# Kernel tuning notes

Measured on AMD Instinct MI355X. Metric: run time of the kernel, lower is better.

The kernel has to match this reference:

```python
import jax, jax.numpy as jnp
import numpy as np

# Static config (matches init_kwargs)
B, T, D = 4, 2048, 1024
E = 8            # num_experts
K = 2            # top_k
S = 1            # num_shared_experts
H = 1408         # expert_hidden_dim = round_to(4*1024//(K+S), 64)
N = B * T        # 8192 tokens
CAPACITY = 2560  # ceil(1.25 * K * N / E)
AUX_COEF = 0.01


def setup_inputs() -> dict:
    key = jax.random.key(0)
    ks = jax.random.split(key, 6)
    s = 1024 ** -0.5
    return {
        "x": jax.random.normal(ks[0], (B, T, D), jnp.float32),
        "router_weight": jax.random.normal(ks[1], (E, D), jnp.float32) * 0.02,
        "w_fc": jax.random.normal(ks[2], (E, D, H), jnp.float32) * s,
        "w_proj": jax.random.normal(ks[3], (E, H, D), jnp.float32) * s,
        "ws_fc": jax.random.normal(ks[4], (S, D, H), jnp.float32) * s,
        "ws_proj": jax.random.normal(ks[5], (S, H, D), jnp.float32) * s,
    }


def reference(x, router_weight, w_fc, w_proj, ws_fc, ws_proj):
    x_flat = x.reshape(N, D)

    # Shared experts: relu(x @ ws_fc)^2 @ ws_proj, summed over S experts
    h_s = jnp.square(jax.nn.relu(jnp.einsum("nd,sdh->snh", x_flat, ws_fc)))
    shared_out = jnp.einsum("snh,shd->nd", h_s, ws_proj)

    # Router: softmax in fp32, top-k, renormalize
    router_logits = x_flat @ router_weight.T                 # [N, E]
    routing_probs = jax.nn.softmax(router_logits.astype(jnp.float32), axis=-1)
    topk_probs, topk_idx = jax.lax.top_k(routing_probs, K)   # [N, K]
    topk_probs = topk_probs / (jnp.sum(topk_probs, axis=-1, keepdims=True) + 1e-9)
    topk_probs = topk_probs.astype(x.dtype)

    # Aux load-balancing loss (f uses top-1 assignment, no grad)
    f = jax.lax.stop_gradient(
        jnp.mean(jax.nn.one_hot(topk_idx[:, 0], E, dtype=routing_probs.dtype), axis=0))
    p = jnp.mean(routing_probs, axis=0)
    aux_loss = AUX_COEF * float(E) * jnp.sum(f * p)

    # Capacity-based dispatch: stable sort assignments by expert id
    flat_idx = topk_idx.reshape(-1)                          # [N*K]
    flat_probs = topk_probs.reshape(-1)                      # [N*K]
    flat_tok = jnp.repeat(jnp.arange(N, dtype=jnp.int32), K)  # [N*K]
    order = jnp.argsort(flat_idx, stable=True)
    sorted_idx = flat_idx[order]
    sorted_tok = flat_tok[order]
    sorted_probs = flat_probs[order]

    counts = jnp.zeros((E,), jnp.int32).at[flat_idx].add(1)
    starts = jnp.concatenate([jnp.zeros((1,), jnp.int32), jnp.cumsum(counts[:-1])])
    pos_within = jnp.arange(N * K, dtype=jnp.int32) - starts[sorted_idx]
    keep = (pos_within < CAPACITY).astype(x.dtype)
    pos_clamped = jnp.minimum(pos_within, CAPACITY - 1)
    slot = sorted_idx * CAPACITY + pos_clamped               # [N*K] -> E*CAPACITY buffer

    # Scatter tokens into per-expert capacity buffers (dropped tokens zeroed by keep)
    expert_inputs = jnp.zeros((E * CAPACITY, D), x.dtype).at[slot].add(
        x_flat[sorted_tok] * keep[:, None])
    expert_inputs = expert_inputs.reshape(E, CAPACITY, D)

    # Grouped expert FFN: relu(.)^2 MLP per expert
    hidden = jnp.square(jax.nn.relu(jnp.einsum("ecd,edh->ech", expert_inputs, w_fc)))
    expert_output = jnp.einsum("ech,ehd->ecd", hidden, w_proj).reshape(E * CAPACITY, D)

    # Gather + weighted scatter-combine back to tokens
    gathered = expert_output[slot]                           # [N*K, D]
    weighted = gathered * (sorted_probs * keep)[:, None]
    routed_out = jnp.zeros((N, D), x.dtype).at[sorted_tok].add(weighted)

    y = (routed_out + shared_out).reshape(B, T, D)
    return y, aux_loss
```

## Files before the change

### kernel.cpp

```cpp
#include <hip/hip_runtime.h>


#define NTOK 8192
#define DDIM 1024
#define HDIM 1408
#define CAP  2560
#define NROWS (NTOK + 8*CAP)
#define YN   8388608

typedef __bf16 bf16x8 __attribute__((ext_vector_type(8)));
typedef float  f32x4  __attribute__((ext_vector_type(4)));

typedef __attribute__((address_space(1))) void gvoid_t;
typedef __attribute__((address_space(3))) void svoid_t;

static __device__ __forceinline__ void load_lds16(const void* g, void* l) {
  __builtin_amdgcn_global_load_lds((gvoid_t*)g, (svoid_t*)l, 16, 0, 0);
}

__global__ __launch_bounds__(256) void zero_kernel(float* __restrict__ y,
                                                   float* __restrict__ psum,
                                                   int* __restrict__ fcnt) {
  size_t idx = (size_t)blockIdx.x * 256 + threadIdx.x;
  float4 z = make_float4(0.f, 0.f, 0.f, 0.f);
  float4* p = (float4*)y;
#pragma unroll
  for (int j = 0; j < 4; ++j) p[idx + (size_t)j * 524288] = z;
  if (idx == 0) {
    y[YN] = 0.f;
    for (int e = 0; e < 8; ++e) { psum[e] = 0.f; fcnt[e] = 0; }
  }
}

__global__ __launch_bounds__(256) void convx_kernel(const float* __restrict__ in,
                                                    __bf16* __restrict__ out) {
  size_t i = ((size_t)blockIdx.x * 256 + threadIdx.x) * 8;
  float4 a = *(const float4*)(in + i);
  float4 b = *(const float4*)(in + i + 4);
  bf16x8 o;
  o[0] = (__bf16)a.x; o[1] = (__bf16)a.y; o[2] = (__bf16)a.z; o[3] = (__bf16)a.w;
  o[4] = (__bf16)b.x; o[5] = (__bf16)b.y; o[6] = (__bf16)b.z; o[7] = (__bf16)b.w;
  *(bf16x8*)(out + i) = o;
}

__global__ __launch_bounds__(256) void tconv_kernel(const float* __restrict__ in,
                                                    __bf16* __restrict__ out, int R, int C) {
  __shared__ float t[32][33];
  size_t mo = (size_t)blockIdx.z * R * C;
  const float* ip = in + mo;
  __bf16* op = out + mo;
  int c0 = blockIdx.x * 32, r0 = blockIdx.y * 32;
  int tx = threadIdx.x, ty = threadIdx.y;
#pragma unroll
  for (int k2 = 0; k2 < 4; ++k2)
    t[ty + k2 * 8][tx] = ip[(size_t)(r0 + ty + k2 * 8) * C + c0 + tx];
  __syncthreads();
#pragma unroll
  for (int k2 = 0; k2 < 4; ++k2)
    op[(size_t)(c0 + ty + k2 * 8) * R + r0 + tx] = (__bf16)t[tx][ty + k2 * 8];
}

__global__ __launch_bounds__(256) void router_kernel(
    const float* __restrict__ x, const float* __restrict__ rw,
    int2* __restrict__ e01, float2* __restrict__ p01,
    int* __restrict__ tok_row, float* __restrict__ scale_row,
    float* __restrict__ psum, int* __restrict__ fcnt) {
  __shared__ float rwl[8 * 1024];
  __shared__ float ps[8];
  __shared__ int fc[8];
  int tid = threadIdx.x;
  if (tid < 8) { ps[tid] = 0.f; fc[tid] = 0; }
  float4* rl4 = (float4*)rwl;
  const float4* rg4 = (const float4*)rw;
#pragma unroll
  for (int j = 0; j < 8; ++j) rl4[tid + 256 * j] = rg4[tid + 256 * j];
  __syncthreads();
  int lane = tid & 63, wid = tid >> 6;
  for (int it = 0; it < 8; ++it) {
    int t = blockIdx.x * 32 + wid * 8 + it;
    const float4* xt = (const float4*)(x + (size_t)t * DDIM);
    float a[8];
#pragma unroll
    for (int e = 0; e < 8; ++e) a[e] = 0.f;
#pragma unroll
    for (int jj = 0; jj < 4; ++jj) {
      float4 v = xt[lane * 4 + jj];
#pragma unroll
      for (int e = 0; e < 8; ++e) {
        float4 w = rl4[e * 256 + lane * 4 + jj];
        a[e] += v.x * w.x + v.y * w.y + v.z * w.z + v.w * w.w;
      }
    }
#pragma unroll
    for (int off = 32; off >= 1; off >>= 1)
#pragma unroll
      for (int e = 0; e < 8; ++e) a[e] += __shfl_xor(a[e], off);
    if (lane == 0) {
      int am = 0; float m = a[0];
      for (int e = 1; e < 8; ++e) if (a[e] > m) { m = a[e]; am = e; }
      float s = 0.f, ex[8];
      for (int e = 0; e < 8; ++e) { ex[e] = expf(a[e] - m); s += ex[e]; }
      float inv = 1.f / s;
      int am2 = -1; float m2 = -3.4e38f;
      for (int e = 0; e < 8; ++e) if (e != am && a[e] > m2) { m2 = a[e]; am2 = e; }
      float p0 = ex[am] * inv, p1 = ex[am2] * inv;
      float rn = 1.f / (p0 + p1 + 1e-9f);
      e01[t] = make_int2(am, am2);
      p01[t] = make_float2(p0 * rn, p1 * rn);
      tok_row[t] = t;
      scale_row[t] = 1.f;
      atomicAdd(&fc[am], 1);
      for (int e = 0; e < 8; ++e) atomicAdd(&ps[e], ex[e] * inv);
    }
  }
  __syncthreads();
  if (tid < 8) { atomicAdd(&psum[tid], ps[tid]); atomicAdd(&fcnt[tid], fc[tid]); }
}

__global__ __launch_bounds__(256) void dispatch_kernel(
    const int2* __restrict__ e01, const float2* __restrict__ p01,
    int* __restrict__ tok_row, float* __restrict__ scale_row, int* __restrict__ counts) {
  __shared__ int lcnt[256][8];
  int tid = threadIdx.x;
  int my[8];
#pragma unroll
  for (int e = 0; e < 8; ++e) my[e] = 0;
  int base = tid * 64;
  for (int j = 0; j < 64; ++j) {
    int ent = base + j; int t = ent >> 1;
    int2 ee = e01[t];
    int ex = (ent & 1) ? ee.y : ee.x;
    my[ex]++;
  }
#pragma unroll
  for (int e = 0; e < 8; ++e) lcnt[tid][e] = my[e];
  __syncthreads();
  if (tid < 8) {
    int run = 0;
    for (int i = 0; i < 256; ++i) { int c = lcnt[i][tid]; lcnt[i][tid] = run; run += c; }
    counts[tid] = run < CAP ? run : CAP;
  }
  __syncthreads();
  int offs[8];
#pragma unroll
  for (int e = 0; e < 8; ++e) offs[e] = lcnt[tid][e];
  for (int j = 0; j < 64; ++j) {
    int ent = base + j; int t = ent >> 1; int k = ent & 1;
    int2 ee = e01[t];
    int ex = k ? ee.y : ee.x;
    float pr = k ? p01[t].y : p01[t].x;
    int pos = offs[ex]++;
    if (pos < CAP) {
      int row = NTOK + ex * CAP + pos;
      tok_row[row] = t;
      scale_row[row] = pr;
    }
  }
}

template <int BM, int BN, int KD, int NDT, int WNV, bool GATHER, int EPI>
__global__ __launch_bounds__(512, 2) void gemm_kernel(
    const __bf16* __restrict__ A, const __bf16* __restrict__ B,
    __bf16* __restrict__ Hout, float* __restrict__ Yout,
    const int* __restrict__ counts, const int* __restrict__ tok_row,
    const float* __restrict__ scale_row) {
  constexpr int NCT = NDT / BN;
  constexpr int T = KD / 32;
  constexpr int AI = BM / 16;
  constexpr int BI = BN / 16;
  constexpr int LI = (AI + BI) / 8;
  constexpr int SH = NTOK / BM;
  constexpr int ET = CAP / BM;
  int nwg = gridDim.x;
  int lin = (blockIdx.x & 7) * (nwg >> 3) + (blockIdx.x >> 3);
  int rem = lin % (4 * NCT);
  int rt = (lin / (4 * NCT)) * 4 + (rem & 3);
  int ct = rem >> 2;

  int g, i0, rowbase;
  if (rt < SH) { g = 8; rowbase = 0; i0 = rt * BM; }
  else { int r = rt - SH; g = r / ET; i0 = (r % ET) * BM; rowbase = NTOK + g * CAP; }
  int cnt = (g == 8) ? NTOK : counts[g];
  if (i0 >= cnt) return;

  __shared__ __align__(16) __bf16 As[4][BM * 32];
  __shared__ __align__(16) __bf16 Bs[4][BN * 32];
  __shared__ int   toksL[BM];
  __shared__ float sclL[BM];

  int tid = threadIdx.x, lane = tid & 63, wid = tid >> 6;

  if (tid < BM) {
    int i = i0 + tid; if (i > cnt - 1) i = cnt - 1;
    toksL[tid] = tok_row[rowbase + i];
    if (EPI == 2) sclL[tid] = scale_row[rowbase + i];
  }
  __syncthreads();

  const char* gsrc[LI];
  int ldsoff[LI];
  bool isA[LI];
  const char* Bg = (const char*)B + (size_t)g * NDT * KD * 2;
#pragma unroll
  for (int q = 0; q < LI; ++q) {
    int j = wid * LI + q;
    int rsub = lane >> 2;
    int chunk = lane & 3;
    if (j < AI) {
      int row = j * 16 + rsub;
      size_t arow = GATHER ? (size_t)toksL[row] : (size_t)(rowbase + i0 + row);
      int csw = chunk ^ ((row >> 1) & 3);
      gsrc[q] = (const char*)A + arow * (size_t)(KD * 2) + csw * 16;
      ldsoff[q] = j * 1024;
      isA[q] = true;
    } else {
      int jb = j - AI;
      int row = jb * 16 + rsub;
      int ib = ct * BN + row;
      int csw = chunk ^ ((row >> 1) & 3);
      gsrc[q] = Bg + (size_t)ib * (KD * 2) + csw * 16;
      ldsoff[q] = jb * 1024;
      isA[q] = false;
    }
  }

  f32x4 acc[4][4];
#pragma unroll
  for (int m2 = 0; m2 < 4; ++m2)
#pragma unroll
    for (int n2 = 0; n2 < 4; ++n2) acc[m2][n2] = f32x4{0.f, 0.f, 0.f, 0.f};

  int wr = wid / WNV, wc = wid % WNV;
  int rdA[4], rdB[4];
#pragma unroll
  for (int m2 = 0; m2 < 4; ++m2) {
    int row = wr * 64 + m2 * 16 + (lane & 15);
    int cs = (lane >> 4) ^ ((row >> 1) & 3);
    rdA[m2] = row * 64 + cs * 16;
  }
#pragma unroll
  for (int n2 = 0; n2 < 4; ++n2) {
    int row = wc * 64 + n2 * 16 + (lane & 15);
    int cs = (lane >> 4) ^ ((row >> 1) & 3);
    rdB[n2] = row * 64 + cs * 16;
  }

  auto stage = [&](int buf, int t) {
#pragma unroll
    for (int q = 0; q < LI; ++q) {
      char* l = (char*)(isA[q] ? &As[buf][0] : &Bs[buf][0]) + ldsoff[q];
      load_lds16(gsrc[q] + (size_t)t * 64, l);
    }
  };
  auto compute = [&](int buf) {
    bf16x8 af[4], bfr[4];
#pragma unroll
    for (int m2 = 0; m2 < 4; ++m2)
      af[m2] = *(const bf16x8*)((const char*)&As[buf][0] + rdA[m2]);
#pragma unroll
    for (int n2 = 0; n2 < 4; ++n2)
      bfr[n2] = *(const bf16x8*)((const char*)&Bs[buf][0] + rdB[n2]);
    __builtin_amdgcn_s_setprio(1);
#pragma unroll
    for (int m2 = 0; m2 < 4; ++m2)
#pragma unroll
      for (int n2 = 0; n2 < 4; ++n2)
        acc[m2][n2] = __builtin_amdgcn_mfma_f32_16x16x32_bf16(af[m2], bfr[n2], acc[m2][n2], 0, 0, 0);
    __builtin_amdgcn_s_setprio(0);
  };
  auto syncstep = [&](int n) {
    if (n == 0)      asm volatile("s_waitcnt vmcnt(0)" ::: "memory");
    else if (n == 3) asm volatile("s_waitcnt vmcnt(3)" ::: "memory");
    else             asm volatile("s_waitcnt vmcnt(6)" ::: "memory");
    __builtin_amdgcn_s_barrier();
    __builtin_amdgcn_sched_barrier(0);
  };

  stage(0, 0);
  stage(1, 1);
  stage(2, 2);
  syncstep(6);
#pragma unroll 4
  for (int t = 0; t < T - 3; ++t) {
    stage((t + 3) & 3, t + 3);
    compute(t & 3);
    syncstep(6);
  }
  compute((T - 3) & 3);
  syncstep(3);
  compute((T - 2) & 3);
  syncstep(0);
  compute((T - 1) & 3);

#pragma unroll
  for (int m2 = 0; m2 < 4; ++m2) {
    int rb = wr * 64 + m2 * 16 + ((lane >> 4) << 2);
#pragma unroll
    for (int n2 = 0; n2 < 4; ++n2) {
      int col = ct * BN + wc * 64 + n2 * 16 + (lane & 15);
#pragma unroll
      for (int r = 0; r < 4; ++r) {
        int grow = i0 + rb + r;
        if (grow < cnt) {
          float v = acc[m2][n2][r];
          if constexpr (EPI == 1) {
            v = fmaxf(v, 0.f);
            Hout[(size_t)(rowbase + grow) * NDT + col] = (__bf16)(v * v);
          } else {
            atomicAdd(&Yout[(size_t)toksL[rb + r] * NDT + col], v * sclL[rb + r]);
          }
        }
      }
    }
  }
}

__global__ void aux_kernel(const float* __restrict__ psum, const int* __restrict__ fcnt,
                           float* __restrict__ out) {
  float s = 0.f;
  for (int e = 0; e < 8; ++e) s += ((float)fcnt[e] / 8192.f) * (psum[e] / 8192.f);
  *out = 0.08f * s;
}

extern "C" void kernel_launch(void* const* d_in, const int* in_sizes, int n_in,
                              void* d_out, int out_size, void* d_ws, size_t ws_size,
                              hipStream_t stream) {
  const float* x      = (const float*)d_in[0];
  const float* rw     = (const float*)d_in[1];
  const float* wfc    = (const float*)d_in[2];
  const float* wproj  = (const float*)d_in[3];
  const float* wsfc   = (const float*)d_in[4];
  const float* wsproj = (const float*)d_in[5];
  float* y = (float*)d_out;

  char* ws = (char*)d_ws;
  size_t off = 0;
  auto alloc = [&](size_t bytes) {
    void* p = ws + off;
    off += (bytes + 1023) & ~(size_t)1023;
    return p;
  };
  __bf16* xbf      = (__bf16*)alloc((size_t)NTOK * DDIM * 2);
  __bf16* B1       = (__bf16*)alloc((size_t)9 * HDIM * DDIM * 2);
  __bf16* B2       = (__bf16*)alloc((size_t)9 * DDIM * HDIM * 2);
  __bf16* H        = (__bf16*)alloc((size_t)NROWS * HDIM * 2);
  int*    tok_row  = (int*)alloc((size_t)NROWS * 4);
  float*  scale_row= (float*)alloc((size_t)NROWS * 4);
  int2*   e01      = (int2*)alloc((size_t)NTOK * 8);
  float2* p01      = (float2*)alloc((size_t)NTOK * 8);
  int*    counts   = (int*)alloc(1024);
  float*  psum     = (float*)alloc(1024);
  int*    fcnt     = (int*)alloc(1024);
  (void)ws_size; (void)out_size; (void)in_sizes; (void)n_in;

  zero_kernel<<<2048, 256, 0, stream>>>(y, psum, fcnt);
  convx_kernel<<<4096, 256, 0, stream>>>(x, xbf);
  dim3 tb(32, 8);
  tconv_kernel<<<dim3(44, 32, 8), tb, 0, stream>>>(wfc, B1, 1024, 1408);
  tconv_kernel<<<dim3(44, 32, 1), tb, 0, stream>>>(wsfc, B1 + (size_t)8 * HDIM * DDIM, 1024, 1408);
  tconv_kernel<<<dim3(32, 44, 8), tb, 0, stream>>>(wproj, B2, 1408, 1024);
  tconv_kernel<<<dim3(32, 44, 1), tb, 0, stream>>>(wsproj, B2 + (size_t)8 * DDIM * HDIM, 1408, 1024);
  router_kernel<<<256, 256, 0, stream>>>(x, rw, e01, p01, tok_row, scale_row, psum, fcnt);
  dispatch_kernel<<<1, 256, 0, stream>>>(e01, p01, tok_row, scale_row, counts);
  gemm_kernel<256, 128, 1024, 1408, 2, true, 1><<<1232, 512, 0, stream>>>(
      xbf, B1, H, nullptr, counts, tok_row, scale_row);
  gemm_kernel<128, 256, 1408, 1024, 4, false, 2><<<896, 512, 0, stream>>>(
      H, B2, nullptr, y, counts, tok_row, scale_row);
  aux_kernel<<<1, 1, 0, stream>>>(psum, fcnt, y + YN);
}
```

Measured before the change: 363.4 us.

## Use 256x256 GEMM tiles and pad expert hidden dim to 1536

Both grouped expert GEMMs now use 256x256 block tiles, with each wave computing a 64x128 sub-tile, so there is more data reuse per LDS load and fewer workgroups. The hidden dimension is padded from 1408 to 1536 so it divides evenly by 256. A new kernel zeroes the padded rows of the first weight matrix, and the transpose kernel gains output stride parameters. The padding adds about 9% extra MFMA work. The larger tiles double LDS per block and the accumulator register count, which may lower occupancy. The padded K columns of the second weight matrix are never initialized, so correctness relies on the zeroed hidden columns multiplying that unset memory without producing NaN.

Result: slower. 387.7 us (+6.7%).

```diff
diff --git a/kernel.cpp b/kernel.cpp
--- a/kernel.cpp
+++ b/kernel.cpp
@@ -4,6 +4,7 @@
 #define NTOK 8192
 #define DDIM 1024
 #define HDIM 1408
+#define HP   1536
 #define CAP  2560
 #define NROWS (NTOK + 8*CAP)
 #define YN   8388608
@@ -30,6 +31,14 @@
     y[YN] = 0.f;
     for (int e = 0; e < 8; ++e) { psum[e] = 0.f; fcnt[e] = 0; }
   }
+}
+
+__global__ __launch_bounds__(256) void zpad_kernel(__bf16* __restrict__ B1) {
+  int idx = blockIdx.x * 256 + threadIdx.x;
+  int e = idx >> 14;
+  int w = idx & 16383;
+  size_t off = (size_t)e * HP * 1024 + (size_t)(HDIM + (w >> 7)) * 1024 + (w & 127) * 8;
+  *(float4*)(B1 + off) = make_float4(0.f, 0.f, 0.f, 0.f);
 }
 
 __global__ __launch_bounds__(256) void convx_kernel(const float* __restrict__ in,
@@ -44,11 +53,11 @@
 }
 
 __global__ __launch_bounds__(256) void tconv_kernel(const float* __restrict__ in,
-                                                    __bf16* __restrict__ out, int R, int C) {
+                                                    __bf16* __restrict__ out,
+                                                    int R, int C, int OS, size_t zs) {
   __shared__ float t[32][33];
-  size_t mo = (size_t)blockIdx.z * R * C;
-  const float* ip = in + mo;
-  __bf16* op = out + mo;
+  const float* ip = in + (size_t)blockIdx.z * R * C;
+  __bf16* op = out + (size_t)blockIdx.z * zs;
   int c0 = blockIdx.x * 32, r0 = blockIdx.y * 32;
   int tx = threadIdx.x, ty = threadIdx.y;
 #pragma unroll
@@ -57,7 +66,7 @@
   __syncthreads();
 #pragma unroll
   for (int k2 = 0; k2 < 4; ++k2)
-    op[(size_t)(c0 + ty + k2 * 8) * R + r0 + tx] = (__bf16)t[tx][ty + k2 * 8];
+    op[(size_t)(c0 + ty + k2 * 8) * OS + r0 + tx] = (__bf16)t[tx][ty + k2 * 8];
 }
 
 __global__ __launch_bounds__(256) void router_kernel(
@@ -158,17 +167,17 @@
   }
 }
 
-template <int BM, int BN, int KD, int NDT, int WNV, bool GATHER, int EPI>
+template <int KD, int NDT, bool GATHER, int EPI>
 __global__ __launch_bounds__(512, 2) void gemm_kernel(
     const __bf16* __restrict__ A, const __bf16* __restrict__ B,
     __bf16* __restrict__ Hout, float* __restrict__ Yout,
     const int* __restrict__ counts, const int* __restrict__ tok_row,
     const float* __restrict__ scale_row) {
+  constexpr int BM = 256, BN = 256;
   constexpr int NCT = NDT / BN;
   constexpr int T = KD / 32;
   constexpr int AI = BM / 16;
-  constexpr int BI = BN / 16;
-  constexpr int LI = (AI + BI) / 8;
+  constexpr int LI = 4;
   constexpr int SH = NTOK / BM;
   constexpr int ET = CAP / BM;
   int nwg = gridDim.x;
@@ -224,14 +233,14 @@
     }
   }
 
-  f32x4 acc[4][4];
+  f32x4 acc[4][8];
 #pragma unroll
   for (int m2 = 0; m2 < 4; ++m2)
 #pragma unroll
-    for (int n2 = 0; n2 < 4; ++n2) acc[m2][n2] = f32x4{0.f, 0.f, 0.f, 0.f};
-
-  int wr = wid / WNV, wc = wid % WNV;
-  int rdA[4], rdB[4];
+    for (int n2 = 0; n2 < 8; ++n2) acc[m2][n2] = f32x4{0.f, 0.f, 0.f, 0.f};
+
+  int wr = wid >> 1, wc = wid & 1;
+  int rdA[4], rdB[8];
 #pragma unroll
   for (int m2 = 0; m2 < 4; ++m2) {
     int row = wr * 64 + m2 * 16 + (lane & 15);
@@ -239,8 +248,8 @@
     rdA[m2] = row * 64 + cs * 16;
   }
 #pragma unroll
-  for (int n2 = 0; n2 < 4; ++n2) {
-    int row = wc * 64 + n2 * 16 + (lane & 15);
+  for (int n2 = 0; n2 < 8; ++n2) {
+    int row = wc * 128 + n2 * 16 + (lane & 15);
     int cs = (lane >> 4) ^ ((row >> 1) & 3);
     rdB[n2] = row * 64 + cs * 16;
   }
@@ -253,25 +262,25 @@
     }
   };
   auto compute = [&](int buf) {
-    bf16x8 af[4], bfr[4];
+    bf16x8 af[4], bfr[8];
 #pragma unroll
     for (int m2 = 0; m2 < 4; ++m2)
       af[m2] = *(const bf16x8*)((const char*)&As[buf][0] + rdA[m2]);
 #pragma unroll
-    for (int n2 = 0; n2 < 4; ++n2)
+    for (int n2 = 0; n2 < 8; ++n2)
       bfr[n2] = *(const bf16x8*)((const char*)&Bs[buf][0] + rdB[n2]);
     __builtin_amdgcn_s_setprio(1);
 #pragma unroll
     for (int m2 = 0; m2 < 4; ++m2)
 #pragma unroll
-      for (int n2 = 0; n2 < 4; ++n2)
+      for (int n2 = 0; n2 < 8; ++n2)
         acc[m2][n2] = __builtin_amdgcn_mfma_f32_16x16x32_bf16(af[m2], bfr[n2], acc[m2][n2], 0, 0, 0);
     __builtin_amdgcn_s_setprio(0);
   };
   auto syncstep = [&](int n) {
     if (n == 0)      asm volatile("s_waitcnt vmcnt(0)" ::: "memory");
-    else if (n == 3) asm volatile("s_waitcnt vmcnt(3)" ::: "memory");
-    else             asm volatile("s_waitcnt vmcnt(6)" ::: "memory");
+    else if (n == 4) asm volatile("s_waitcnt vmcnt(4)" ::: "memory");
+    else             asm volatile("s_waitcnt vmcnt(8)" ::: "memory");
     __builtin_amdgcn_s_barrier();
     __builtin_amdgcn_sched_barrier(0);
   };
@@ -279,15 +288,15 @@
   stage(0, 0);
   stage(1, 1);
   stage(2, 2);
-  syncstep(6);
+  syncstep(8);
 #pragma unroll 4
   for (int t = 0; t < T - 3; ++t) {
     stage((t + 3) & 3, t + 3);
     compute(t & 3);
-    syncstep(6);
+    syncstep(8);
   }
   compute((T - 3) & 3);
-  syncstep(3);
+  syncstep(4);
   compute((T - 2) & 3);
   syncstep(0);
   compute((T - 1) & 3);
@@ -296,8 +305,8 @@
   for (int m2 = 0; m2 < 4; ++m2) {
     int rb = wr * 64 + m2 * 16 + ((lane >> 4) << 2);
 #pragma unroll
-    for (int n2 = 0; n2 < 4; ++n2) {
-      int col = ct * BN + wc * 64 + n2 * 16 + (lane & 15);
+    for (int n2 = 0; n2 < 8; ++n2) {
+      int col = ct * BN + wc * 128 + n2 * 16 + (lane & 15);
 #pragma unroll
       for (int r = 0; r < 4; ++r) {
         int grow = i0 + rb + r;
@@ -341,9 +350,9 @@
     return p;
   };
   __bf16* xbf      = (__bf16*)alloc((size_t)NTOK * DDIM * 2);
-  __bf16* B1       = (__bf16*)alloc((size_t)9 * HDIM * DDIM * 2);
-  __bf16* B2       = (__bf16*)alloc((size_t)9 * DDIM * HDIM * 2);
-  __bf16* H        = (__bf16*)alloc((size_t)NROWS * HDIM * 2);
+  __bf16* B1       = (__bf16*)alloc((size_t)9 * HP * DDIM * 2);
+  __bf16* B2       = (__bf16*)alloc((size_t)9 * DDIM * HP * 2);
+  __bf16* H        = (__bf16*)alloc((size_t)NROWS * HP * 2);
   int*    tok_row  = (int*)alloc((size_t)NROWS * 4);
   float*  scale_row= (float*)alloc((size_t)NROWS * 4);
   int2*   e01      = (int2*)alloc((size_t)NTOK * 8);
@@ -354,17 +363,18 @@
   (void)ws_size; (void)out_size; (void)in_sizes; (void)n_in;
 
   zero_kernel<<<2048, 256, 0, stream>>>(y, psum, fcnt);
+  zpad_kernel<<<576, 256, 0, stream>>>(B1);
   convx_kernel<<<4096, 256, 0, stream>>>(x, xbf);
   dim3 tb(32, 8);
-  tconv_kernel<<<dim3(44, 32, 8), tb, 0, stream>>>(wfc, B1, 1024, 1408);
-  tconv_kernel<<<dim3(44, 32, 1), tb, 0, stream>>>(wsfc, B1 + (size_t)8 * HDIM * DDIM, 1024, 1408);
-  tconv_kernel<<<dim3(32, 44, 8), tb, 0, stream>>>(wproj, B2, 1408, 1024);
-  tconv_kernel<<<dim3(32, 44, 1), tb, 0, stream>>>(wsproj, B2 + (size_t)8 * DDIM * HDIM, 1408, 1024);
+  tconv_kernel<<<dim3(44, 32, 8), tb, 0, stream>>>(wfc, B1, 1024, 1408, 1024, (size_t)HP * 1024);
+  tconv_kernel<<<dim3(44, 32, 1), tb, 0, stream>>>(wsfc, B1 + (size_t)8 * HP * 1024, 1024, 1408, 1024, (size_t)HP * 1024);
+  tconv_kernel<<<dim3(32, 44, 8), tb, 0, stream>>>(wproj, B2, 1408, 1024, HP, (size_t)1024 * HP);
+  tconv_kernel<<<dim3(32, 44, 1), tb, 0, stream>>>(wsproj, B2 + (size_t)8 * 1024 * HP, 1408, 1024, HP, (size_t)1024 * HP);
   router_kernel<<<256, 256, 0, stream>>>(x, rw, e01, p01, tok_row, scale_row, psum, fcnt);
   dispatch_kernel<<<1, 256, 0, stream>>>(e01, p01, tok_row, scale_row, counts);
-  gemm_kernel<256, 128, 1024, 1408, 2, true, 1><<<1232, 512, 0, stream>>>(
+  gemm_kernel<1024, HP, true, 1><<<672, 512, 0, stream>>>(
       xbf, B1, H, nullptr, counts, tok_row, scale_row);
-  gemm_kernel<128, 256, 1408, 1024, 4, false, 2><<<896, 512, 0, stream>>>(
+  gemm_kernel<HP, 1024, false, 2><<<448, 512, 0, stream>>>(
       H, B2, nullptr, y, counts, tok_row, scale_row);
   aux_kernel<<<1, 1, 0, stream>>>(psum, fcnt, y + YN);
 }
```
